# Kernel optimization log

Hardware: AMD Instinct MI355X
Metric: run time of the kernel (lower is better)

## Reference

```python
import jax, jax.numpy as jnp
import numpy as np

WINDOW = 32


def _dilate(mask, iters=5):
    # scipy binary_dilation with default cross structure, `iters` iterations
    m = mask.copy()
    for _ in range(iters):
        d = m.copy()
        d[1:, :] |= m[:-1, :]
        d[:-1, :] |= m[1:, :]
        d[:, 1:] |= m[:, :-1]
        d[:, :-1] |= m[:, 1:]
        m = d
    return m


def _label8(mask):
    # skimage measure.label, default 8-connectivity, via min-label propagation
    h, w = mask.shape
    lab = np.where(mask, np.arange(1, mask.size + 1, dtype=np.int64).reshape(h, w), 0)
    BIG = mask.size + 2
    while True:
        p = np.pad(np.where(mask, lab, BIG), 1, constant_values=BIG)
        m = np.full((h, w), BIG, dtype=np.int64)
        for dy in (-1, 0, 1):
            for dx in (-1, 0, 1):
                m = np.minimum(m, p[1 + dy:1 + dy + h, 1 + dx:1 + dx + w])
        new = np.where(mask, m, 0)
        if np.array_equal(new, lab):
            break
        lab = new
    u = np.unique(lab)
    out = np.searchsorted(u, lab)
    if u[0] != 0:
        out = out + 1
    return out


def _malis(seg_flat, e1, e2, costs, pos):
    # MALIS edge weights: Kruskal on descending affinities with union-find;
    # pos=True counts same-(nonzero)-label pairs merged by each edge,
    # pos=False counts cross-label pairs between labeled nodes.
    n = seg_flat.size
    parent = np.arange(n)
    cnt = [dict() for _ in range(n)]
    for i in range(n):
        s = int(seg_flat[i])
        if s != 0:
            cnt[i][s] = 1
    w = np.zeros(costs.shape[0], np.float32)

    def find(x):
        r = x
        while parent[r] != r:
            r = parent[r]
        while parent[x] != r:
            parent[x], x = r, parent[x]
        return r

    order = np.argsort(-costs, kind='stable')
    for ei in order:
        ra, rb = find(int(e1[ei])), find(int(e2[ei]))
        if ra == rb:
            continue
        ca, cb = cnt[ra], cnt[rb]
        small, large = (ca, cb) if len(ca) <= len(cb) else (cb, ca)
        same = 0
        for kk, v in small.items():
            same += v * large.get(kk, 0)
        if pos:
            w[ei] = same
        else:
            sa = sum(ca.values())
            sb = sum(cb.values())
            w[ei] = sa * sb - same
        parent[rb] = ra
        for kk, v in cb.items():
            ca[kk] = ca.get(kk, 0) + v
        cnt[rb] = None
    return w


def compute_malis_weights(pred_np, target_np):
    B, C, H, W = pred_np.shape
    wn_full = np.zeros(pred_np.shape, np.float32)
    wp_full = np.zeros(pred_np.shape, np.float32)
    win = WINDOW
    idx = np.arange(win * win).reshape(win, win)
    e1 = np.concatenate([idx[:, :-1].ravel(), idx[:-1, :].ravel()])
    e2 = np.concatenate([idx[:, 1:].ravel(), idx[1:, :].ravel()])
    for k in range(H // win):
        for j in range(W // win):
            p = pred_np[:, :, k * win:(k + 1) * win, j * win:(j + 1) * win]
            t = target_np[:, :, k * win:(k + 1) * win, j * win:(j + 1) * win]
            costs = np.concatenate([
                (p[:, :, :, :-1] + p[:, :, :, 1:]).reshape(B, -1),
                (p[:, :, :-1, :] + p[:, :, 1:, :]).reshape(B, -1)], axis=1).astype(np.float32)
            gtc = np.concatenate([
                (t[:, :, :, :-1] + t[:, :, :, 1:]).reshape(B, -1),
                (t[:, :, :-1, :] + t[:, :, 1:, :]).reshape(B, -1)], axis=1).astype(np.float32)
            costs_n = costs.copy()
            costs_p = costs.copy()
            costs_n[gtc > 20] = 20
            costs_p[gtc < 10] = 0
            gtc = np.minimum(gtc, 20)
            for i in range(B):
                sg = _label8(_dilate(t[i, 0] == 0, 5) == 0)
                en = _malis(sg.ravel(), e1, e2, costs_n[i], False)
                ep = _malis(sg.ravel(), e1, e2, costs_p[i], True)
                sn = en.sum()
                if sn > 0:
                    en = en / sn
                sp = ep.sum()
                if sp > 0:
                    ep = ep / sp
                en[gtc[i] >= 10] = 0
                ep[gtc[i] < 20] = 0
                for ew, out in ((en, wn_full), (ep, wp_full)):
                    wh, wv = np.split(ew, 2)
                    wh = wh.reshape(win, win - 1)
                    wv = wv.reshape(win - 1, win)
                    nodes = np.zeros((win, win), np.float32)
                    nodes[:, :-1] += wh
                    nodes[:, 1:] += wh
                    nodes[:-1, :] += wv
                    nodes[1:, :] += wv
                    out[i, 0, k * win:(k + 1) * win, j * win:(j + 1) * win] = nodes
    return wn_full, wp_full


def setup_inputs() -> dict:
    key = jax.random.key(0)
    k1, k2 = jax.random.split(key)
    pred = jax.random.uniform(k1, (2, 1, 256, 256), jnp.float32) * 20.0
    target = jax.random.randint(k2, (2, 1, 256, 256), 0, 26).astype(jnp.float32)
    return {"pred": pred, "target": target, "malis_lr": 1.0, "malis_lr_pos": 1.0}


def reference(pred, target, malis_lr, malis_lr_pos):
    # weights are computed from detached values (CPU graph algorithm), constants wrt autodiff
    wn, wp = compute_malis_weights(np.asarray(pred), np.asarray(target))
    wn = jnp.asarray(wn, jnp.float32)
    wp = jnp.asarray(wp, jnp.float32)
    loss = malis_lr * jnp.square(pred) * wn + malis_lr_pos * jnp.square(20.0 - pred) * wp
    return loss.sum()
```

## Files before the change

### kernel.cpp

```cpp
#include <hip/hip_runtime.h>
#include <cstdint>

#define NPIX  1024
#define NH    992
#define NEDGE 1984
#define NSORT 2048
#define NGRP  31
#define HFS   4300
#define POOLN (NPIX + 2*HFS)

typedef unsigned long long u64;
typedef unsigned int u32;

static __device__ __forceinline__ u64 packRoot(int sL,int off,int len,int cap){
    return (u64)(u32)(sL & 0x7FF) | ((u64)(u32)(off & 0x3FFF) << 11) |
           ((u64)(u32)(len & 0x7FF) << 25) | ((u64)(u32)(cap & 0x7FF) << 36);
}
#define R_SL(R)  ((int)((R) & 0x7FF))
#define R_OFF(R) ((int)(((R)>>11) & 0x3FFF))
#define R_LEN(R) ((int)(((R)>>25) & 0x7FF))
#define R_CAP(R) ((int)(((R)>>36) & 0x7FF))
#define EMASK 0x3FFFFFFu

static __device__ __forceinline__ int rdl(int v, int l){ return __builtin_amdgcn_readlane(v, l); }

static __device__ __forceinline__ u64 sxor64(u64 v, int m){
    u32 lo = (u32)__shfl_xor((int)(v & 0xFFFFFFFFull), m, 64);
    u32 hi = (u32)__shfl_xor((int)(v >> 32), m, 64);
    return ((u64)hi << 32) | lo;
}

static __device__ __forceinline__ void edgeAB(int e, int &a, int &b){
    if (e < NH) { int r = (int)((unsigned)e / 31u); a = e + r; b = a + 1; }
    else        { a = e - NH; b = a + 32; }
}

static __device__ __forceinline__ int winBase(int wslot){
    int bb = wslot >> 6;
    int win = wslot & 63;
    int wy = win >> 3, wx = win & 7;
    return bb * 65536 + (wy * 32) * 256 + wx * 32;
}

#define CE(x, y, up) { u64 _a=(x), _b=(y); bool _lt=(_a<_b); \
    u64 _mn=_lt?_a:_b, _mx=_lt?_b:_a; (x)=(up)?_mn:_mx; (y)=(up)?_mx:_mn; }
#define CEX(x, xm, keepmin) { u64 _p=sxor64((x),(xm)); bool _lt=((x)<_p); \
    u64 _mn=_lt?(x):_p, _mx=_lt?_p:(x); (x)=(keepmin)?_mn:_mx; }

static __device__ __forceinline__ int wredi(int v){
    #pragma unroll
    for (int o = 32; o > 0; o >>= 1) v += __shfl_xor(v, o, 64);
    return v;
}
static __device__ __forceinline__ float wredf(float v){
    #pragma unroll
    for (int o = 32; o > 0; o >>= 1) v += __shfl_xor(v, o, 64);
    return v;
}

__global__ __launch_bounds__(64) void malis_kernel(
    const float* __restrict__ pred,
    const float* __restrict__ target,
    const float* __restrict__ lr_p,
    const float* __restrict__ lrp_p,
    float* __restrict__ out)
{
    const int lane = threadIdx.x;
    const int bid  = blockIdx.x;
    const int ph   = bid & 1;
    const int wslot= bid >> 1;
    const int base = winBase(wslot);
    const u64 ltm = (1ull << lane) - 1;

    __shared__ __align__(16) u32 Ks_[NSORT];
    __shared__ u64   root_[NPIX];
    __shared__ u32   pool_[POOLN];
    __shared__ unsigned short Q_[NPIX];
    __shared__ float Qw_[NPIX];
    __shared__ u32   claim_[NPIX];
    __shared__ short par_[NPIX];
    __shared__ short H_[NPIX + 1];
    __shared__ float predL[NPIX];
    __shared__ float costs[NEDGE];
    __shared__ short seg[NPIX];
    __shared__ unsigned char tgtL[NPIX];
    __shared__ unsigned char gtcL[NEDGE];
    __shared__ u32   rowmaskL[32];
    __shared__ u32   fgL[32];
    __shared__ unsigned short baseL[33];

    u32* runPar = (u32*)pool_;
    unsigned short* labIdRun = (unsigned short*)(runPar + 512);

    for (int j = 0; j < 16; ++j) {
        int i = lane + 64 * j;
        int r = (j << 1) + (lane >> 5), c = lane & 31;
        float pv = pred[base + r * 256 + c];
        float tv = target[base + r * 256 + c];
        predL[i] = pv;
        tgtL[i]  = (unsigned char)tv;
        u64 zb = __ballot(tv == 0.0f);
        if (lane == 0) {
            rowmaskL[2*j]     = (u32)zb;
            rowmaskL[2*j + 1] = (u32)(zb >> 32);
        }
    }
    for (int x = lane; x < 512; x += 64) runPar[x] = (u32)x;
    __builtin_amdgcn_wave_barrier();

    if (lane < 32) {
        u32 m = rowmaskL[lane];
        #pragma unroll
        for (int it = 0; it < 5; ++it) {
            u32 um = __shfl(m, (lane == 0) ? 0 : lane - 1, 64);
            if (lane == 0) um = 0;
            u32 dm = __shfl(m, (lane == 31) ? 31 : lane + 1, 64);
            if (lane == 31) dm = 0;
            m = m | (m << 1) | (m >> 1) | um | dm;
        }
        u32 f = ~m;
        fgL[lane] = f;
        int ns = __popc(f & ~(f << 1));
        int x = ns;
        #pragma unroll
        for (int off = 1; off < 32; off <<= 1) {
            int y = __shfl(x, (lane >= off) ? lane - off : 0, 64);
            if (lane >= off) x += y;
        }
        baseL[lane] = (unsigned short)(x - ns);
        if (lane == 31) baseL[32] = (unsigned short)x;
    }
    __builtin_amdgcn_wave_barrier();
    const int nRuns = (int)baseL[32];

    for (;;) {
        bool chg = false;
        for (int j = 0; j < 16; ++j) {
            int i = lane + 64 * j;
            int r = i >> 5, c = i & 31;
            if (r == 0) continue;
            u32 fr = fgL[r];
            if (!((fr >> c) & 1u)) continue;
            u32 fu = fgL[r - 1];
            u32 nb = fu & (u32)((7ull << c) >> 1);
            if (!nb) continue;
            u32 Sr = fr & ~(fr << 1);
            int a = (int)baseL[r] + __popc(Sr & ((2u << c) - 1u)) - 1;
            for (;;) { int p = (int)runPar[a]; if (p == a) break; a = p; }
            u32 Su = fu & ~(fu << 1);
            int bu = (int)baseL[r - 1];
            while (nb) {
                int cc = __ffs((int)nb) - 1; nb &= nb - 1;
                int b = bu + __popc(Su & ((2u << cc) - 1u)) - 1;
                for (;;) { int p = (int)runPar[b]; if (p == b) break; b = p; }
                if (a != b) {
                    int mnr = a < b ? a : b;
                    int mxr = a ^ b ^ mnr;
                    atomicMin(&runPar[mxr], (u32)mnr);
                    chg = true;
                    a = mnr;
                }
            }
        }
        if (!__ballot(chg)) break;
        for (int x = lane; x < nRuns; x += 64) {
            u32 p = runPar[x];
            runPar[x] = runPar[p];
        }
        __builtin_amdgcn_wave_barrier();
    }

    {
        int kacc = 0;
        for (int x0 = 0; x0 < nRuns; x0 += 64) {
            int x = x0 + lane;
            bool isr = (x < nRuns) && ((int)runPar[x] == x);
            u64 bm = __ballot(isr);
            if (isr) labIdRun[x] = (unsigned short)(kacc + (int)__popcll(bm & ltm));
            kacc += (int)__popcll(bm);
        }
    }
    __builtin_amdgcn_wave_barrier();

    for (int j = 0; j < 16; ++j) {
        int i = lane + 64 * j;
        int r = i >> 5, c = i & 31;
        u32 fr = fgL[r];
        short s = 0;
        if ((fr >> c) & 1u) {
            u32 Sr = fr & ~(fr << 1);
            int x = (int)baseL[r] + __popc(Sr & ((2u << c) - 1u)) - 1;
            for (;;) { int p = (int)runPar[x]; if (p == x) break; x = p; }
            s = (short)((int)labIdRun[x] + 1);
        }
        seg[i] = s;
    }

    for (int e = lane; e < NEDGE; e += 64) {
        int a, b2; edgeAB(e, a, b2);
        costs[e] = predL[a] + predL[b2];
        gtcL[e]  = (unsigned char)(tgtL[a] + tgtL[b2]);
    }
    __builtin_amdgcn_wave_barrier();

    u64 sk[32];
    #pragma unroll
    for (int r = 0; r < 32; ++r) {
        int e = lane * 32 + r;
        u64 kv = ~0ULL;
        if (e < NEDGE) {
            float cv = costs[e];
            int g = gtcL[e];
            if (ph == 0) { if (g > 20) cv = 20.0f; }
            else         { if (g < 10) cv = 0.0f; }
            kv = (((u64)(~__float_as_uint(cv))) << 32) | (u32)e;
        }
        sk[r] = kv;
    }
    #pragma unroll
    for (int kk2 = 2; kk2 <= 32; kk2 <<= 1) {
        #pragma unroll
        for (int j = kk2 >> 1; j > 0; j >>= 1) {
            #pragma unroll
            for (int r = 0; r < 32; ++r) {
                if ((r & j) == 0) {
                    bool up = (kk2 == 32) ? ((lane & 1) == 0) : ((r & kk2) == 0);
                    CE(sk[r], sk[r | j], up);
                }
            }
        }
    }
    #pragma unroll
    for (int kk2 = 64; kk2 <= 2048; kk2 <<= 1) {
        const bool up = ((lane & (kk2 >> 5)) == 0);
        #pragma unroll
        for (int j = kk2 >> 1; j >= 32; j >>= 1) {
            const int xm = j >> 5;
            const bool keepmin = (((lane & xm) == 0) == up);
            #pragma unroll
            for (int r = 0; r < 32; ++r) { CEX(sk[r], xm, keepmin); }
        }
        #pragma unroll
        for (int j = 16; j > 0; j >>= 1) {
            #pragma unroll
            for (int r = 0; r < 32; ++r) {
                if ((r & j) == 0) { CE(sk[r], sk[r | j], up); }
            }
        }
    }
    #pragma unroll
    for (int r = 0; r < 32; r += 4) {
        uint4 v4;
        v4.x = (u32)sk[r]; v4.y = (u32)sk[r+1]; v4.z = (u32)sk[r+2]; v4.w = (u32)sk[r+3];
        *(uint4*)&Ks_[lane * 32 + r] = v4;
    }

    for (int i = lane; i < NPIX; i += 64) {
        short s2 = seg[i];
        par_[i] = (short)(i | (s2 ? 0x8000 : 0));
        root_[i] = s2 ? ((1ull << 62) | ((u32)(unsigned short)s2 << 16) | 1u) : 0ull;
        H_[i] = 0;
        claim_[i] = ~0u;
    }
    if (lane == 0) H_[NPIX] = 0;
    __builtin_amdgcn_wave_barrier();

    u32 bump = NPIX;
    u32 halfEnd = NPIX + HFS;
    int curHalf = 0;

    auto do_gc = [&]() {
        u32 tgt = (curHalf == 0) ? (u32)(NPIX + HFS) : (u32)NPIX;
        u32 nb = tgt;
        for (int c = 0; c < 16; ++c) {
            int i0 = c * 64 + lane;
            u64 Ri = root_[i0];
            bool live = (Ri != 0) && ((Ri >> 62) == 0);
            u64 rbm = __ballot(live);
            while (rbm) {
                int j = __ffsll(rbm) - 1; rbm &= rbm - 1;
                int r = c * 64 + j;
                u64 R = root_[r];
                int len = R_LEN(R);
                int off = R_OFF(R);
                for (int t = lane; t < len; t += 64) {
                    u32 v2 = pool_[off + t];
                    pool_[nb + t] = v2;
                }
                __builtin_amdgcn_wave_barrier();
                if (lane == 0) root_[r] = packRoot(R_SL(R), (int)nb, len, len);
                nb += (u32)len;
            }
        }
        bump = nb;
        halfEnd = tgt + HFS;
        curHalf ^= 1;
    };

    int qn = 0;
    u32 rnd = 1;
    int curE = (int)Ks_[lane];
    for (int g2 = 0; g2 < NGRP; ++g2) {
        int nextE = (g2 + 1 < NGRP) ? (int)Ks_[(g2 + 1) * 64 + lane] : 0;
        const int myE = curE;
        int ea, eb2; edgeAB(myE, ea, eb2);
        int ra = ea, rb = eb2;
        int laA, laB;
        for (;;) {
            int va = (int)(unsigned short)par_[ra];
            int vb = (int)(unsigned short)par_[rb];
            int pa = va & 0x3FF, pb = vb & 0x3FF;
            bool fa = (pa != ra), fb = (pb != rb);
            if (!fa && !fb) { laA = va >> 15; laB = vb >> 15; break; }
            int ga = (int)(unsigned short)par_[pa];
            int gb = (int)(unsigned short)par_[pb];
            if (fa) { par_[ra] = (short)ga; ra = ga & 0x3FF; }
            if (fb) { par_[rb] = (short)gb; rb = gb & 0x3FF; }
        }
        bool alive = (ra != rb);

        for (;;) {
            if (!__ballot(alive)) break;
            const bool av = alive;
            const u32 tag = ((0x03FFFFFFu - rnd) << 6) | (u32)lane;
            ++rnd;
            int mn = ra < rb ? ra : rb;
            int mx = ra ^ rb ^ mn;
            int winner = (laA == laB) ? mn : (laA ? ra : rb);
            int loser  = (laA == laB) ? mx : (laA ? rb : ra);
            bool wgt = (laA & laB) != 0;
            if (av)        atomicMin(&claim_[loser],  tag);
            if (av && wgt) atomicMin(&claim_[winner], tag);
            bool sel = false;
            if (av) {
                u32 cl = claim_[loser];
                u32 cw = wgt ? claim_[winner] : tag;
                sel = (cl == tag) && (cw == tag);
            }
            u64 wm = __ballot(sel && wgt);
            int qidx = qn + (int)__popcll(wm & ltm);
            qn += (int)__popcll(wm);
            if (sel) par_[loser] = (short)winner;

            bool needPool = false;
            if (sel && wgt) {
                u64 RW = root_[mn], RL = root_[mx];
                int tW = (int)(RW >> 62), tL2 = (int)(RL >> 62);
                if (tW != 0 && tL2 != 0) {
                    u32 a0 = (u32)RW & EMASK, a1 = (u32)(RW >> 26) & EMASK;
                    u32 b0 = (u32)RL & EMASK, b1 = (u32)(RL >> 26) & EMASK;
                    u32 la0 = a0 >> 16, la1 = a1 >> 16;
                    u32 lb0 = b0 >> 16, lb1 = b1 >> 16;
                    int ca0 = (int)(a0 & 0xFFFF), ca1 = (int)(a1 & 0xFFFF);
                    int cb0 = (int)(b0 & 0xFFFF), cb1 = (int)(b1 & 0xFFFF);
                    int sLa = ca0 + ((tW == 2) ? ca1 : 0);
                    int sLb = cb0 + ((tL2 == 2) ? cb1 : 0);
                    int same = 0;
                    if (lb0 == la0) same += ca0 * cb0;
                    else if (tW == 2 && lb0 == la1) same += ca1 * cb0;
                    if (tL2 == 2) {
                        if (lb1 == la0) same += ca0 * cb1;
                        else if (tW == 2 && lb1 == la1) same += ca1 * cb1;
                    }
                    u32 r0 = a0, r1 = (tW == 2) ? a1 : 0;
                    int n = tW; bool ovf = false;
                    if (lb0 == la0) r0 += (u32)cb0;
                    else if (tW == 2 && lb0 == la1) r1 += (u32)cb0;
                    else { if (n == 1) { r1 = b0; n = 2; } else ovf = true; }
                    if (tL2 == 2) {
                        if (lb1 == la0) r0 += (u32)cb1;
                        else if (tW == 2 && lb1 == la1) r1 += (u32)cb1;
                        else { if (n == 1) { r1 = b1; n = 2; } else ovf = true; }
                    }
                    if (!ovf) {
                        root_[mn] = ((u64)(u32)n << 62) | ((u64)r1 << 26) | r0;
                        root_[mx] = 0;
                        Qw_[qidx] = (float)(ph ? same : (sLa * sLb - same));
                        Q_[qidx]  = (unsigned short)myE;
                    } else needPool = true;
                } else needPool = true;
            }

            u64 pm = __ballot(needPool);
            while (pm) {
                int f = __ffsll(pm) - 1; pm &= pm - 1;
                int A  = rdl(mn, f),  B  = rdl(mx, f);
                int e  = rdl(myE, f), qi = rdl(qidx, f);
                u64 RA = root_[A], RB = root_[B];
                int tA = (int)(RA >> 62), tB = (int)(RB >> 62);
                int lenA = tA ? tA : R_LEN(RA);
                int lenB = tB ? tB : R_LEN(RB);
                if (bump + (u32)(lenA + lenB + 8) > halfEnd) {
                    do_gc();
                    RA = root_[A]; RB = root_[B];
                    tA = (int)(RA >> 62); tB = (int)(RB >> 62);
                    lenA = tA ? tA : R_LEN(RA);
                    lenB = tB ? tB : R_LEN(RB);
                }
                int sLa, sLb;
                int offA = 0, capA = 0, offB = 0, capB = 0;
                if (tA == 0) { sLa = R_SL(RA); offA = R_OFF(RA); capA = R_CAP(RA); }
                else {
                    u32 a0 = (u32)RA & EMASK, a1 = (u32)(RA >> 26) & EMASK;
                    sLa = (int)(a0 & 0xFFFF) + ((tA == 2) ? (int)(a1 & 0xFFFF) : 0);
                }
                if (tB == 0) { sLb = R_SL(RB); offB = R_OFF(RB); capB = R_CAP(RB); }
                else {
                    u32 b0 = (u32)RB & EMASK, b1 = (u32)(RB >> 26) & EMASK;
                    sLb = (int)(b0 & 0xFFFF) + ((tB == 2) ? (int)(b1 & 0xFFFF) : 0);
                }
                u32 eA = 0, eB = 0;
                if (lenA <= 64) {
                    if (tA == 0) { if (lane < lenA) eA = pool_[offA + lane]; }
                    else {
                        u32 a0 = (u32)RA & EMASK, a1 = (u32)(RA >> 26) & EMASK;
                        eA = (lane == 0) ? a0 : ((lane == 1 && tA == 2) ? a1 : 0);
                    }
                }
                if (lenB <= 64) {
                    if (tB == 0) { if (lane < lenB) eB = pool_[offB + lane]; }
                    else {
                        u32 b0 = (u32)RB & EMASK, b1 = (u32)(RB >> 26) & EMASK;
                        eB = (lane == 0) ? b0 : ((lane == 1 && tB == 2) ? b1 : 0);
                    }
                }
                u32 eS, eL; int lenS, lenL, offS, offL, capL, tL;
                if (lenA <= lenB) { eS=eA; lenS=lenA; offS=offA; eL=eB; lenL=lenB; offL=offB; capL=capB; tL=tB; }
                else              { eS=eB; lenS=lenB; offS=offB; eL=eA; lenL=lenA; offL=offA; capL=capA; tL=tA; }
                int dOff, dLen, dCap;
                int same = 0;
                u64 newR;

                if (lenS + lenL <= 64) {
                    dLen = lenL;
                    for (int t = 0; t < lenS; ++t) {
                        u32 xs = (u32)rdl((int)eS, t);
                        bool match = (lane < lenL) && ((eL >> 16) == (xs >> 16));
                        u64 mb = __ballot(match);
                        if (mb) {
                            int ml = __ffsll(mb) - 1;
                            same += (int)(xs & 0xFFFF) * ((int)rdl((int)eL, ml) & 0xFFFF);
                            if (match) eL += (xs & 0xFFFF);
                        } else {
                            if (lane == dLen) eL = xs;
                            dLen++;
                        }
                    }
                    if (dLen <= 2) {
                        u32 m0 = (u32)rdl((int)eL, 0) & EMASK;
                        u32 m1 = (dLen > 1) ? ((u32)rdl((int)eL, 1) & EMASK) : 0u;
                        newR = ((u64)(u32)dLen << 62) | ((u64)m1 << 26) | m0;
                    } else {
                        if (tL == 0 && dLen <= capL) { dOff = offL; dCap = capL; }
                        else { dOff = (int)bump; dCap = (dLen + 3) & ~3; bump += (u32)dCap; }
                        if (lane < dLen) pool_[dOff + lane] = eL;
                        newR = packRoot(sLa + sLb, dOff, dLen, dCap);
                    }
                } else {
                    dOff = (int)bump;
                    dCap = (lenL + lenS + 4) & ~3; bump += (u32)dCap;
                    if (lenS <= 64) {
                        if (lane < lenS) H_[eS >> 16] = (short)(eS & 0xFFFF);
                    } else {
                        for (int j = lane; j < lenS; j += 64) {
                            u32 es = pool_[offS + j];
                            H_[es >> 16] = (short)(es & 0xFFFF);
                        }
                    }
                    __builtin_amdgcn_wave_barrier();
                    int sp = 0;
                    for (int j = lane; j < lenL; j += 64) {
                        u32 el = pool_[offL + j];
                        int h = (int)H_[el >> 16];
                        sp += h * (int)(el & 0xFFFF);
                        pool_[dOff + j] = el + (u32)h;
                        if (h) H_[el >> 16] = 0;
                    }
                    same = wredi(sp);
                    __builtin_amdgcn_wave_barrier();
                    int baseU = 0;
                    if (lenS <= 64) {
                        bool un = (lane < lenS) && (H_[eS >> 16] != 0);
                        u64 ub = __ballot(un);
                        if (un) {
                            int pos = __popcll(ub & ltm);
                            pool_[dOff + lenL + pos] = eS;
                            H_[eS >> 16] = 0;
                        }
                        baseU = (int)__popcll(ub);
                    } else {
                        for (int j0 = 0; j0 < lenS; j0 += 64) {
                            int j = j0 + lane;
                            bool un = false; u32 es = 0;
                            if (j < lenS) { es = pool_[offS + j]; un = (H_[es >> 16] != 0); }
                            u64 ub = __ballot(un);
                            if (un) {
                                int pos = __popcll(ub & ltm);
                                pool_[dOff + lenL + baseU + pos] = es;
                                H_[es >> 16] = 0;
                            }
                            baseU += (int)__popcll(ub);
                        }
                    }
                    dLen = lenL + baseU;
                    newR = packRoot(sLa + sLb, dOff, dLen, dCap);
                }
                if (lane == 0) {
                    Qw_[qi] = (float)(ph ? same : (sLa * sLb - same));
                    Q_[qi]  = (unsigned short)e;
                    root_[A] = newR;
                    root_[B] = 0;
                }
                __builtin_amdgcn_wave_barrier();
            }

            if (av) {
                for (;;) {
                    int va = (int)(unsigned short)par_[ra];
                    int vb = (int)(unsigned short)par_[rb];
                    int pa = va & 0x3FF, pb = vb & 0x3FF;
                    bool fa = (pa != ra), fb = (pb != rb);
                    if (!fa && !fb) { laA = va >> 15; laB = vb >> 15; break; }
                    int ga = (int)(unsigned short)par_[pa];
                    int gb = (int)(unsigned short)par_[pb];
                    if (fa) { par_[ra] = (short)ga; ra = ga & 0x3FF; }
                    if (fb) { par_[rb] = (short)gb; rb = gb & 0x3FF; }
                }
                alive = !sel && (ra != rb);
            }
        }
        curE = nextE;
        __builtin_amdgcn_wave_barrier();
    }

    float s_loc = 0.0f;
    for (int q = lane; q < qn; q += 64) s_loc += Qw_[q];
    const float sn = wredf(s_loc);

    const float scale = ph ? lrp_p[0] : lr_p[0];
    float acc = 0.0f;
    for (int q = lane; q < qn; q += 64) {
        float wv2 = Qw_[q];
        if (wv2 == 0.0f) continue;
        if (sn > 0.0f) wv2 /= sn;
        int me = (int)Q_[q];
        int g = gtcL[me];
        bool zero = ph ? (g < 20) : (g >= 10);
        if (zero) continue;
        int a2, b2; edgeAB(me, a2, b2);
        float pa = predL[a2], pb = predL[b2];
        float fa2, fb2;
        if (ph == 0) { fa2 = pa * pa; fb2 = pb * pb; }
        else { float qa = 20.0f - pa, qb = 20.0f - pb; fa2 = qa * qa; fb2 = qb * qb; }
        acc += scale * wv2 * (fa2 + fb2);
    }
    acc = wredf(acc);
    if (lane == 0) atomicAdd(out, acc);
}

__global__ void zero_out_kernel(float* o)
{
    if (threadIdx.x == 0 && blockIdx.x == 0) o[0] = 0.0f;
}

extern "C" void kernel_launch(void* const* d_in, const int* in_sizes, int n_in,
                              void* d_out, int out_size, void* d_ws, size_t ws_size,
                              hipStream_t stream)
{
    const float* pred   = (const float*)d_in[0];
    const float* target = (const float*)d_in[1];
    const float* lr     = (const float*)d_in[2];
    const float* lrp    = (const float*)d_in[3];
    float* out = (float*)d_out;

    zero_out_kernel<<<1, 64, 0, stream>>>(out);
    malis_kernel<<<256, 64, 0, stream>>>(pred, target, lr, lrp, out);
}
```

Measured before the change: 323.9 us.

## Batch same-label single-entry merges into one winner root per round

Adds a second claim array so that several lanes whose edges merge single-label components of the same label into one shared winner root can all commit in the same round. Their counts are combined with a lane-ordered prefix sum over readlanes, so each edge's positive weight follows Kruskal order within the group. Before, each round let at most one lane claim a given winner, which serialized long chains of merges into the same large component. In exchange it adds extra atomics, a second shared array, and a per-group readlane scan loop. It also risks subtle ordering errors if the group semantics do not match the sequential edge order.

```diff
diff --git a/kernel.cpp b/kernel.cpp
--- a/kernel.cpp
+++ b/kernel.cpp
@@ -78,6 +78,7 @@
     __shared__ unsigned short Q_[NPIX];
     __shared__ float Qw_[NPIX];
     __shared__ u32   claim_[NPIX];
+    __shared__ u32   blockClaim_[NPIX];
     __shared__ short par_[NPIX];
     __shared__ short H_[NPIX + 1];
     __shared__ float predL[NPIX];
@@ -261,6 +262,7 @@
         root_[i] = s2 ? ((1ull << 62) | ((u32)(unsigned short)s2 << 16) | 1u) : 0ull;
         H_[i] = 0;
         claim_[i] = ~0u;
+        blockClaim_[i] = ~0u;
     }
     if (lane == 0) H_[NPIX] = 0;
     __builtin_amdgcn_wave_barrier();
@@ -322,29 +324,77 @@
         for (;;) {
             if (!__ballot(alive)) break;
             const bool av = alive;
-            const u32 tag = ((0x03FFFFFFu - rnd) << 6) | (u32)lane;
+            const u32 tagBase = (0x03FFFFFFu - rnd) << 6;
+            const u32 tag = tagBase | (u32)lane;
             ++rnd;
             int mn = ra < rb ? ra : rb;
             int mx = ra ^ rb ^ mn;
             int winner = (laA == laB) ? mn : (laA ? ra : rb);
             int loser  = (laA == laB) ? mx : (laA ? rb : ra);
             bool wgt = (laA & laB) != 0;
-            if (av)        atomicMin(&claim_[loser],  tag);
-            if (av && wgt) atomicMin(&claim_[winner], tag);
-            bool sel = false;
+
+            u64 RW = 0, RL = 0;
+            if (av && wgt) { RW = root_[mn]; RL = root_[mx]; }
+            u32 ew0 = (u32)RW & EMASK, el0 = (u32)RL & EMASK;
+            bool elig = av && wgt && ((RW >> 62) == 1ull) && ((RL >> 62) == 1ull)
+                        && ((ew0 >> 16) == (el0 >> 16));
+
+            if (av)          atomicMin(&claim_[loser],  tag);
+            if (av && wgt) { atomicMin(&claim_[winner], tag);
+                             atomicMin(&blockClaim_[loser], tag); }
+            if (av && wgt && !elig) atomicMin(&blockClaim_[winner], tag);
+
+            bool go = false;
             if (av) {
-                u32 cl = claim_[loser];
-                u32 cw = wgt ? claim_[winner] : tag;
-                sel = (cl == tag) && (cw == tag);
-            }
-            u64 wm = __ballot(sel && wgt);
+                u32 lc = claim_[loser];
+                bool selL = (lc == tag);
+                if (!wgt) go = selL;
+                else {
+                    u32 wc = claim_[winner];
+                    u32 bw = blockClaim_[winner];
+                    int blockMin = ((bw & ~63u) == tagBase) ? (int)(bw & 63u) : 64;
+                    go = selL && (elig ? (lane < blockMin) : (wc == tag));
+                }
+            }
+            u64 wm = __ballot(go && wgt);
             int qidx = qn + (int)__popcll(wm & ltm);
             qn += (int)__popcll(wm);
-            if (sel) par_[loser] = (short)winner;
+            if (go) par_[loser] = (short)winner;
+
+            u64 scanB = __ballot(go && elig);
+            int cWv = (int)(ew0 & 0xFFFF);
+            int cbv = (int)(el0 & 0xFFFF);
+            if (scanB) {
+                u64 pend = scanB;
+                while (pend) {
+                    int l0 = __ffsll(pend) - 1;
+                    int w0 = rdl(mn, l0);
+                    bool inC = (((scanB >> lane) & 1ull) != 0) && (mn == w0);
+                    u64 mk = __ballot(inC);
+                    pend &= ~mk;
+                    int cW0 = rdl(cWv, l0);
+                    int pre = 0, tot = 0;
+                    u64 t = mk;
+                    while (t) {
+                        int li = __ffsll(t) - 1; t &= t - 1;
+                        int cbi = rdl(cbv, li);
+                        if (li < lane) pre += cbi;
+                        tot += cbi;
+                    }
+                    if (inC) {
+                        int sLaEff = cW0 + pre;
+                        Qw_[qidx] = ph ? (float)(sLaEff * cbv) : 0.0f;
+                        Q_[qidx]  = (unsigned short)myE;
+                        root_[mx] = 0;
+                        if (lane == 63 - __clzll(mk))
+                            root_[mn] = (1ull << 62) |
+                                (u64)((ew0 & 0x3FF0000u) | (u32)(cW0 + tot));
+                    }
+                }
+            }
 
             bool needPool = false;
-            if (sel && wgt) {
-                u64 RW = root_[mn], RL = root_[mx];
+            if (go && wgt && !elig) {
                 int tW = (int)(RW >> 62), tL2 = (int)(RL >> 62);
                 if (tW != 0 && tL2 != 0) {
                     u32 a0 = (u32)RW & EMASK, a1 = (u32)(RW >> 26) & EMASK;
@@ -526,7 +576,7 @@
                     if (fa) { par_[ra] = (short)ga; ra = ga & 0x3FF; }
                     if (fb) { par_[rb] = (short)gb; rb = gb & 0x3FF; }
                 }
-                alive = !sel && (ra != rb);
+                alive = !go && (ra != rb);
             }
         }
         curE = nextE;
```

Measured after the change: 347.9 us. 1.07x slower.
